# Kernel tuning notes

Hardware: AMD Instinct MI355X
Metric: run time of the kernel (lower is better)

The kernel has to match this reference:

```python
import jax, jax.numpy as jnp
import numpy as np

B, N, D = 4, 1024, 1024   # batch, seq (x and context must match), model dim
H, DH = 16, 64            # heads, dim_head; inner_dim = H*DH = 1024
INNER = H * DH
EPS = 1e-5


def setup_inputs() -> dict:
    key = jax.random.key(0)
    ks = jax.random.split(key, 12)
    s = 0.02
    return {
        "x": jax.random.normal(ks[0], (B, N, D), dtype=jnp.float32),
        "context": jax.random.normal(ks[1], (B, N, D), dtype=jnp.float32),
        # weights stored as [in, out] (torch Linear weight transposed)
        "W_qk": jax.random.normal(ks[2], (D, INNER), dtype=jnp.float32) * s,
        "W_cqk": jax.random.normal(ks[3], (D, INNER), dtype=jnp.float32) * s,
        "W_v": jax.random.normal(ks[4], (D, INNER), dtype=jnp.float32) * s,
        "W_cv": jax.random.normal(ks[5], (D, INNER), dtype=jnp.float32) * s,
        "W_out": jax.random.normal(ks[6], (INNER, D), dtype=jnp.float32) * s,
        "b_out": jax.random.normal(ks[7], (D,), dtype=jnp.float32) * s,
        "W_cout": jax.random.normal(ks[8], (INNER, D), dtype=jnp.float32) * s,
        "b_cout": jax.random.normal(ks[9], (D,), dtype=jnp.float32) * s,
        "gamma": jnp.ones((D,), dtype=jnp.float32),
        "beta": jnp.zeros((D,), dtype=jnp.float32),
    }


def _split_heads(t):  # [b, n, h*d] -> [b, h, n, d]
    b, n, _ = t.shape
    return t.reshape(b, n, H, DH).transpose(0, 2, 1, 3)


def _merge_heads(t):  # [b, h, n, d] -> [b, n, h*d]
    b, h, n, d = t.shape
    return t.transpose(0, 2, 1, 3).reshape(b, n, h * d)


def _layernorm(y, gamma, beta):
    mu = jnp.mean(y, axis=-1, keepdims=True)
    var = jnp.var(y, axis=-1, keepdims=True)
    return gamma * (y - mu) * jax.lax.rsqrt(var + EPS) + beta


def reference(x, context, W_qk, W_cqk, W_v, W_cv, W_out, b_out, W_cout, b_cout, gamma, beta):
    scale = DH ** -0.5
    res = x + context                       # residual (requires identical shapes)
    # prenorm=False -> identity norms; dropout=0; talking_heads=False -> identity
    qk = _split_heads(x @ W_qk)             # [b,h,i,d]
    v = _split_heads(x @ W_v)               # [b,h,i,d]
    cqk = _split_heads(context @ W_cqk)     # [b,h,j,d]
    cv = _split_heads(context @ W_cv)       # [b,h,j,d]

    sim = jnp.einsum('bhid,bhjd->bhij', qk, cqk) * scale  # shared similarity
    attn = jax.nn.softmax(sim, axis=-1)      # row softmax (x attends to context)
    context_attn = jax.nn.softmax(sim, axis=-2)  # column softmax (context attends to x)

    out = jnp.einsum('bhij,bhjd->bhid', attn, cv)          # [b,h,i,d]
    context_out = jnp.einsum('bhji,bhjd->bhid', context_attn, v)  # [b,h,i,d]

    out = _merge_heads(out) @ W_out + b_out
    context_out = _merge_heads(context_out) @ W_cout + b_cout
    return _layernorm(out + context_out, gamma, beta) + res
```

## Files before the change

kernel.cpp:

```cpp
#include <hip/hip_runtime.h>
#include <hip/hip_bf16.h>

typedef unsigned short u16;
typedef __bf16 bf16x8 __attribute__((ext_vector_type(8)));
typedef float   f32x4 __attribute__((ext_vector_type(4)));
typedef u16     u16x8 __attribute__((ext_vector_type(8)));
typedef u16     u16x4 __attribute__((ext_vector_type(4)));

#define DEV static __device__ __forceinline__

DEV float bf2f(u16 b) { unsigned int u = ((unsigned int)b) << 16; return __builtin_bit_cast(float, u); }
DEV u16   f2bf(float f) { return __builtin_bit_cast(u16, (__bf16)f); }
DEV bf16x8 ldb(const u16* p) { return __builtin_bit_cast(bf16x8, *(const u16x8*)p); }

DEV f32x4 mfma_bf16(bf16x8 a, bf16x8 b, f32x4 c) {
  return __builtin_amdgcn_mfma_f32_16x16x32_bf16(a, b, c, 0, 0, 0);
}

DEV void gl16(const u16* g, u16* l) {
  __builtin_amdgcn_global_load_lds((const __attribute__((address_space(1))) unsigned int*)g,
                                   (__attribute__((address_space(3))) unsigned int*)l,
                                   16, 0, 0);
}

#define BAR_VM4()  asm volatile("s_waitcnt vmcnt(4)\ns_barrier" ::: "memory")
#define BAR_VM0()  asm volatile("s_waitcnt vmcnt(0)\ns_barrier" ::: "memory")
#define BAR_LG()   asm volatile("s_waitcnt lgkmcnt(0)\ns_barrier" ::: "memory")
#define BAR_FULL() asm volatile("s_waitcnt vmcnt(0) lgkmcnt(0)\ns_barrier" ::: "memory")

__global__ __launch_bounds__(256) void detect_dtype(const u16* x, int* flag) {
  int tid = threadIdx.x;
  u16 lo = x[tid * 2];
  float v = bf2f(lo);
  float av = fabsf(v);
  bool plaus = (av > 1e-4f && av < 50.f);
  __shared__ int cnt;
  if (tid == 0) cnt = 0;
  __syncthreads();
  if (plaus) atomicAdd(&cnt, 1);
  __syncthreads();
  if (tid == 0) *flag = (cnt >= 128) ? 1 : 0;
}

struct Cv2 { const void* s[2]; u16* d[2]; };
__global__ __launch_bounds__(256) void convert_big(Cv2 p, const int* flagp) {
  int fl = *flagp;
  const void* src = p.s[blockIdx.z];
  u16* dst = p.d[blockIdx.z];
  size_t i = ((size_t)blockIdx.x * 256 + threadIdx.x) * 8;
  if (fl) {
    *(u16x8*)(dst + i) = *(const u16x8*)((const u16*)src + i);
  } else {
    const float* s = (const float*)src + i;
    u16x8 o;
#pragma unroll
    for (int k = 0; k < 8; ++k) o[k] = f2bf(s[k]);
    *(u16x8*)(dst + i) = o;
  }
}

struct Sm4 { const void* s[4]; u16* d[4]; };
__global__ __launch_bounds__(256) void convert_smalls(Sm4 p, const int* flagp) {
  int fl = *flagp;
  const void* src = p.s[blockIdx.x];
  u16* dst = p.d[blockIdx.x];
  int i = threadIdx.x * 4;
#pragma unroll
  for (int k = 0; k < 4; ++k)
    dst[i + k] = fl ? ((const u16*)src)[i + k] : f2bf(((const float*)src)[i + k]);
}

struct T6 { const void* s[6]; u16* d[6]; };

__global__ __launch_bounds__(256) void transpose6(T6 t, const int* flagp) {
  int fl = *flagp;
  __shared__ u16 tile[64 * 72];
  const void* src = t.s[blockIdx.z];
  u16* dst = t.d[blockIdx.z];
  int x0 = blockIdx.x * 64, y0 = blockIdx.y * 64;
  int tid = threadIdx.x;
  int r8 = tid >> 3, ch = tid & 7;

#pragma unroll
  for (int half = 0; half < 2; ++half) {
    int rl = r8 + half * 32;
    size_t si = (size_t)(y0 + rl) * 1024 + x0 + ch * 8;
    u16x8 v;
    if (fl) {
      v = *(const u16x8*)((const u16*)src + si);
    } else {
      const float* s = (const float*)src + si;
      float4 a = *(const float4*)s, b2 = *(const float4*)(s + 4);
      v[0]=f2bf(a.x); v[1]=f2bf(a.y); v[2]=f2bf(a.z); v[3]=f2bf(a.w);
      v[4]=f2bf(b2.x); v[5]=f2bf(b2.y); v[6]=f2bf(b2.z); v[7]=f2bf(b2.w);
    }
    int pr = rl ^ (ch << 3);
#pragma unroll
    for (int k = 0; k < 8; ++k)
      tile[(ch * 8 + k) * 72 + pr] = v[k];
  }
  __syncthreads();
#pragma unroll
  for (int half = 0; half < 2; ++half) {
    int dr = r8 + half * 32;
    int pch = ch ^ ((dr >> 3) & 7);
    u16x8 v = *(const u16x8*)(tile + dr * 72 + pch * 8);
    *(u16x8*)(dst + (size_t)(x0 + dr) * 1024 + y0 + ch * 8) = v;
  }
}

struct Proj4 { const u16* A[4]; const u16* Bt[4]; u16* C[4]; int mode[4]; };

__global__ __launch_bounds__(512, 2) void gemm_proj(Proj4 p) {
  const int K = 1024, Nn = 1024;
  const u16* A  = p.A[blockIdx.z];
  const u16* Bt = p.Bt[blockIdx.z];
  u16* C = p.C[blockIdx.z];
  int mode = p.mode[blockIdx.z];

  __shared__ __align__(16) u16 As[2][256 * 64];
  __shared__ __align__(16) u16 Bs[2][256 * 64];

  int tid = threadIdx.x, lane = tid & 63, w = tid >> 6;
  int wm = w >> 2, wn = w & 3;
  int q4 = lane >> 4, c = lane & 15;

  int bid = blockIdx.y * 4 + blockIdx.x;
  int wg  = (bid & 7) * 8 + (bid >> 3);
  int m0 = (wg >> 2) * 256, n0 = (wg & 3) * 256;

  int srow = w * 8 + (lane >> 3);
  int scol = ((lane & 7) ^ (lane >> 3)) * 8;
  const u16* pAg = A  + (size_t)(m0 + srow) * K + scol;
  const u16* pBg = Bt + (size_t)(n0 + srow) * K + scol;
  int sdst = (w * 8) * 64;

  int xo0 = ((0 * 4 + q4) ^ (c & 7)) * 8;
  int xo1 = ((1 * 4 + q4) ^ (c & 7)) * 8;

  f32x4 acc[8][4] = {};

#define STAGE256(pb, kt)                                                    \
  { int ko = (kt) * 64;                                                     \
    _Pragma("unroll") for (int s = 0; s < 4; ++s) {                         \
      gl16(pAg + (size_t)s * 64 * 1024 + ko, As[pb] + s * 4096 + sdst);     \
      gl16(pBg + (size_t)s * 64 * 1024 + ko, Bs[pb] + s * 4096 + sdst);     \
    } }

#define COMP256(pb)                                                         \
  { bf16x8 bq[4][2];                                                        \
    _Pragma("unroll") for (int j = 0; j < 4; ++j) {                         \
      int rb = (wn * 64 + j * 16 + c) * 64;                                 \
      bq[j][0] = ldb(Bs[pb] + rb + xo0);                                    \
      bq[j][1] = ldb(Bs[pb] + rb + xo1);                                    \
    }                                                                       \
    _Pragma("unroll") for (int f = 0; f < 4; ++f) {                         \
      bf16x8 aq[2][2];                                                      \
      _Pragma("unroll") for (int ii = 0; ii < 2; ++ii) {                    \
        int ra = (wm * 128 + (f * 2 + ii) * 16 + c) * 64;                   \
        aq[ii][0] = ldb(As[pb] + ra + xo0);                                 \
        aq[ii][1] = ldb(As[pb] + ra + xo1);                                 \
      }                                                                     \
      __builtin_amdgcn_s_setprio(1);                                        \
      _Pragma("unroll") for (int ii = 0; ii < 2; ++ii)                      \
        _Pragma("unroll") for (int j = 0; j < 4; ++j) {                     \
          acc[f*2+ii][j] = mfma_bf16(aq[ii][0], bq[j][0], acc[f*2+ii][j]);  \
          acc[f*2+ii][j] = mfma_bf16(aq[ii][1], bq[j][1], acc[f*2+ii][j]);  \
        }                                                                   \
      __builtin_amdgcn_s_setprio(0);                                        \
    } }

  STAGE256(0, 0);
  BAR_VM0();
  for (int t = 0; t < 16; t += 2) {
    STAGE256(1, t + 1);
    COMP256(0);
    BAR_FULL();
    if (t + 2 < 16) STAGE256(0, t + 2);
    COMP256(1);
    BAR_FULL();
  }
#undef STAGE256
#undef COMP256

  if (mode == 0) {
#pragma unroll
    for (int i = 0; i < 8; ++i) {
      int mrow = m0 + wm * 128 + i * 16 + q4 * 4;
#pragma unroll
      for (int j = 0; j < 4; ++j) {
        int col = n0 + wn * 64 + j * 16 + c;
#pragma unroll
        for (int r = 0; r < 4; ++r)
          C[(size_t)(mrow + r) * Nn + col] = f2bf(acc[i][j][r]);
      }
    }
  } else {
    int bidx = m0 >> 10;
#pragma unroll
    for (int i = 0; i < 8; ++i) {
      int mrow = m0 + wm * 128 + i * 16 + q4 * 4;
      int jj = mrow & 1023;
#pragma unroll
      for (int j = 0; j < 4; ++j) {
        int col = n0 + wn * 64 + j * 16 + c;
        int h = col >> 6, dh = col & 63;
        u16x4 pk;
#pragma unroll
        for (int r = 0; r < 4; ++r) pk[r] = f2bf(acc[i][j][r]);
        *(u16x4*)(C + ((size_t)((bidx * 16 + h) * 64 + dh)) * 1024 + jj) = pk;
      }
    }
  }
}

struct FAz { const u16* Q[2]; const u16* Kp[2]; const u16* Vp[2]; u16* O[2]; };

__global__ __launch_bounds__(256) void flash_attn(FAz fa) {
  int flat = blockIdx.x;
  int i0 = (flat >> 7) * 128;
  int grp = flat & 127;
  int z = grp >> 6;
  int bh = grp & 63;
  const u16* Q  = fa.Q[z];
  const u16* Kg = fa.Kp[z];
  const u16* Vt = fa.Vp[z];
  u16* O = fa.O[z];

  int b = bh >> 4, h = bh & 15;
  int tid = threadIdx.x, lane = tid & 63, w = tid >> 6;
  int q4 = lane >> 4, c = lane & 15;

  __shared__ __align__(16) u16 Ks[64 * 64];
  __shared__ __align__(16) u16 Vs[64 * 64];
  __shared__ __align__(16) u16 Ps[4][2][16 * 72];

  bf16x8 qf[2][2];
#pragma unroll
  for (int g = 0; g < 2; ++g) {
    const size_t qoff = ((size_t)(b * 1024 + i0 + g * 64 + w * 16 + c)) * 1024 + h * 64 + q4 * 8;
    qf[g][0] = ldb(Q + qoff);
    qf[g][1] = ldb(Q + qoff + 32);
  }

  f32x4 of[2][4] = {};
  f32x4 lacc[2] = {};
  bf16x8 ones;
#pragma unroll
  for (int k = 0; k < 8; ++k) ones[k] = (__bf16)1.0f;

  int jr = tid >> 2, seg = (tid & 3) * 16;
  const u16* krow_base = Kg + ((size_t)(b * 1024 + jr)) * 1024 + h * 64 + seg;
  const u16* vrow_base = Vt + ((size_t)((b * 16 + h) * 64 + jr)) * 1024 + seg;

  int ch0 = (tid & 3) * 2, jrx = jr & 7;
  int wa0 = jr * 64 + ((ch0)     ^ jrx) * 8;
  int wa1 = jr * 64 + ((ch0 + 1) ^ jrx) * 8;
  int xA = (q4 ^ (c & 7)) * 8;
  int xB = xA ^ 32;

  const float C2 = 0.125f * 1.4426950408889634f;

  u16x8 kv0 = *(const u16x8*)(krow_base);
  u16x8 kv1 = *(const u16x8*)(krow_base + 8);
  u16x8 vv0 = *(const u16x8*)(vrow_base);
  u16x8 vv1 = *(const u16x8*)(vrow_base + 8);

  for (int j0 = 0; j0 < 1024; j0 += 64) {
    __syncthreads();
    *(u16x8*)(Ks + wa0) = kv0;
    *(u16x8*)(Ks + wa1) = kv1;
    *(u16x8*)(Vs + wa0) = vv0;
    *(u16x8*)(Vs + wa1) = vv1;
    __syncthreads();

    if (j0 + 64 < 1024) {
      const u16* ks = krow_base + (size_t)(j0 + 64) * 1024;
      kv0 = *(const u16x8*)(ks);
      kv1 = *(const u16x8*)(ks + 8);
      const u16* vs = vrow_base + j0 + 64;
      vv0 = *(const u16x8*)(vs);
      vv1 = *(const u16x8*)(vs + 8);
    }

    f32x4 sf[2][4] = {};
    __builtin_amdgcn_s_setprio(1);
#pragma unroll
    for (int jc = 0; jc < 4; ++jc) {
      int rk = (jc * 16 + c) * 64;
      bf16x8 k0f = ldb(Ks + rk + xA);
      bf16x8 k1f = ldb(Ks + rk + xB);
#pragma unroll
      for (int g = 0; g < 2; ++g) {
        sf[g][jc] = mfma_bf16(k0f, qf[g][0], sf[g][jc]);
        sf[g][jc] = mfma_bf16(k1f, qf[g][1], sf[g][jc]);
      }
    }
    __builtin_amdgcn_s_setprio(0);

#pragma unroll
    for (int g = 0; g < 2; ++g)
#pragma unroll
      for (int jc = 0; jc < 4; ++jc) {
        u16x4 pk;
#pragma unroll
        for (int r = 0; r < 4; ++r)
          pk[r] = f2bf(__builtin_amdgcn_exp2f(sf[g][jc][r] * C2));
        *(u16x4*)(Ps[w][g] + c * 72 + jc * 16 + q4 * 4) = pk;
      }

    asm volatile("s_waitcnt lgkmcnt(0)" ::: "memory");

    bf16x8 pf[2][2];
#pragma unroll
    for (int g = 0; g < 2; ++g) {
      pf[g][0] = ldb(Ps[w][g] + c * 72 + q4 * 8);
      pf[g][1] = ldb(Ps[w][g] + c * 72 + 32 + q4 * 8);
      lacc[g] = mfma_bf16(pf[g][0], ones, lacc[g]);
      lacc[g] = mfma_bf16(pf[g][1], ones, lacc[g]);
    }

    __builtin_amdgcn_s_setprio(1);
#pragma unroll
    for (int dc = 0; dc < 4; ++dc) {
      int rv = (dc * 16 + c) * 64;
      bf16x8 v0f = ldb(Vs + rv + xA);
      bf16x8 v1f = ldb(Vs + rv + xB);
#pragma unroll
      for (int g = 0; g < 2; ++g) {
        of[g][dc] = mfma_bf16(pf[g][0], v0f, of[g][dc]);
        of[g][dc] = mfma_bf16(pf[g][1], v1f, of[g][dc]);
      }
    }
    __builtin_amdgcn_s_setprio(0);
  }

#pragma unroll
  for (int g = 0; g < 2; ++g) {
    float inv[4];
#pragma unroll
    for (int r = 0; r < 4; ++r) inv[r] = 1.0f / lacc[g][r];
#pragma unroll
    for (int dc = 0; dc < 4; ++dc) {
      int col = h * 64 + dc * 16 + c;
#pragma unroll
      for (int r = 0; r < 4; ++r) {
        int irow = i0 + g * 64 + w * 16 + q4 * 4 + r;
        O[((size_t)(b * 1024 + irow)) * 1024 + col] = f2bf(of[g][dc][r] * inv[r]);
      }
    }
  }
}

__global__ __launch_bounds__(256) void gemm_final(const u16* A1, const u16* B1t,
                                                  const u16* A2, const u16* B2t,
                                                  const u16* b1, const u16* b2,
                                                  float* Y) {
  const int K = 1024, Nn = 1024;
  __shared__ __align__(16) u16 As[2][128 * 32];
  __shared__ __align__(16) u16 Bs[2][128 * 32];

  int tid = threadIdx.x, lane = tid & 63, w = tid >> 6;
  int wm = w & 1, wn = w >> 1;
  int q4 = lane >> 4, c = lane & 15;

  int bid = blockIdx.y * 8 + blockIdx.x;
  int wg  = (bid & 7) * 32 + (bid >> 3);
  int m0 = (wg >> 3) * 128, n0 = (wg & 7) * 128;

  int r0 = w * 32 + (lane >> 2);
  int cc = (lane & 3) ^ ((lane >> 3) & 3);
  const u16* A1p = A1  + (size_t)(m0 + r0) * K + cc * 8;
  const u16* A2p = A2  + (size_t)(m0 + r0) * K + cc * 8;
  const u16* B1p = B1t + (size_t)(n0 + r0) * K + cc * 8;
  const u16* B2p = B2t + (size_t)(n0 + r0) * K + cc * 8;
  int qs = (q4 ^ ((c >> 1) & 3)) * 8;

  f32x4 acc[4][4] = {};

#define STAGE_F(buf, kk)                                          \
  { const u16* Ap = ((kk) < 32) ? A1p : A2p;                      \
    const u16* Bp = ((kk) < 32) ? B1p : B2p;                      \
    int k0_ = ((kk) & 31) * 32;                                   \
    gl16(Ap + k0_,          As[buf] + w * 1024);                  \
    gl16(Ap + 16 * K + k0_, As[buf] + w * 1024 + 512);            \
    gl16(Bp + k0_,          Bs[buf] + w * 1024);                  \
    gl16(Bp + 16 * K + k0_, Bs[buf] + w * 1024 + 512); }

#define COMP_F(buf)                                               \
  { bf16x8 af[4], bfr[4];                                         \
    _Pragma("unroll") for (int i = 0; i < 4; ++i)                 \
      af[i]  = ldb(As[buf] + (wm * 64 + i * 16 + c) * 32 + qs);   \
    _Pragma("unroll") for (int j = 0; j < 4; ++j)                 \
      bfr[j] = ldb(Bs[buf] + (wn * 64 + j * 16 + c) * 32 + qs);   \
    _Pragma("unroll") for (int i = 0; i < 4; ++i)                 \
      _Pragma("unroll") for (int j = 0; j < 4; ++j)               \
        acc[i][j] = mfma_bf16(af[i], bfr[j], acc[i][j]); }

  STAGE_F(0, 0);
  for (int t = 0; t < 62; t += 2) {
    STAGE_F(1, t + 1);
    BAR_VM4();
    COMP_F(0);
    BAR_LG();
    STAGE_F(0, t + 2);
    BAR_VM4();
    COMP_F(1);
    BAR_LG();
  }
  STAGE_F(1, 63);
  BAR_VM4();
  COMP_F(0);
  BAR_LG();
  BAR_VM0();
  COMP_F(1);
#undef STAGE_F
#undef COMP_F

#pragma unroll
  for (int i = 0; i < 4; ++i) {
    int mrow = m0 + wm * 64 + i * 16 + q4 * 4;
#pragma unroll
    for (int j = 0; j < 4; ++j) {
      int col = n0 + wn * 64 + j * 16 + c;
      float bias = bf2f(b1[col]) + bf2f(b2[col]);
#pragma unroll
      for (int r = 0; r < 4; ++r)
        Y[(size_t)(mrow + r) * Nn + col] = acc[i][j][r] + bias;
    }
  }
}

__global__ __launch_bounds__(256) void ln_res(const float* Y, const u16* gamma, const u16* beta,
                                              const void* x, const void* ctx, void* out,
                                              const int* flagp) {
  int fl = *flagp;
  int row = blockIdx.x;
  int tid = threadIdx.x;
  const float* y = Y + (size_t)row * 1024;
  float4 v = *(const float4*)(y + tid * 4);
  float s  = v.x + v.y + v.z + v.w;
  float s2 = v.x * v.x + v.y * v.y + v.z * v.z + v.w * v.w;
#pragma unroll
  for (int off = 1; off < 64; off <<= 1) { s += __shfl_xor(s, off); s2 += __shfl_xor(s2, off); }
  __shared__ float red[8];
  int w = tid >> 6, lane = tid & 63;
  if (lane == 0) { red[w] = s; red[w + 4] = s2; }
  __syncthreads();
  float S  = red[0] + red[1] + red[2] + red[3];
  float S2 = red[4] + red[5] + red[6] + red[7];
  float mu  = S * (1.0f / 1024.0f);
  float var = S2 * (1.0f / 1024.0f) - mu * mu;
  float rs = rsqrtf(var + 1e-5f);
  size_t base = (size_t)row * 1024 + tid * 4;
  u16x4 gv = *(const u16x4*)(gamma + tid * 4);
  u16x4 bv = *(const u16x4*)(beta + tid * 4);
  float xr[4], cr[4];
  if (fl) {
    u16x4 xv = *(const u16x4*)((const u16*)x + base);
    u16x4 cv = *(const u16x4*)((const u16*)ctx + base);
#pragma unroll
    for (int k = 0; k < 4; ++k) { xr[k] = bf2f(xv[k]); cr[k] = bf2f(cv[k]); }
  } else {
    float4 xv = *(const float4*)((const float*)x + base);
    float4 cv = *(const float4*)((const float*)ctx + base);
    xr[0] = xv.x; xr[1] = xv.y; xr[2] = xv.z; xr[3] = xv.w;
    cr[0] = cv.x; cr[1] = cv.y; cr[2] = cv.z; cr[3] = cv.w;
  }
  float vv[4] = {v.x, v.y, v.z, v.w};
  float o[4];
#pragma unroll
  for (int k = 0; k < 4; ++k)
    o[k] = bf2f(gv[k]) * (vv[k] - mu) * rs + bf2f(bv[k]) + xr[k] + cr[k];
  if (fl) {
    u16x4 ov;
#pragma unroll
    for (int k = 0; k < 4; ++k) ov[k] = f2bf(o[k]);
    *(u16x4*)((u16*)out + base) = ov;
  } else {
    *(float4*)((float*)out + base) = make_float4(o[0], o[1], o[2], o[3]);
  }
}

__global__ __launch_bounds__(256) void sentinel(u16* out) {
  size_t i = ((size_t)blockIdx.x * 256 + threadIdx.x) * 8;
  u16 v = f2bf(12345.0f);
  u16x8 o = {v, v, v, v, v, v, v, v};
  *(u16x8*)(out + i) = o;
}

extern "C" void kernel_launch(void* const* d_in, const int* in_sizes, int n_in,
                              void* d_out, int out_size, void* d_ws, size_t ws_size,
                              hipStream_t stream) {
  (void)in_sizes; (void)n_in; (void)out_size;
  const size_t MB = 1024 * 1024;
  const size_t NEED = 61 * MB;
  if (ws_size < NEED) {
    sentinel<<<2048, 256, 0, stream>>>((u16*)d_out);
    return;
  }

  char* ws = (char*)d_ws;
  u16* wt[6];
  for (int i = 0; i < 6; ++i) wt[i] = (u16*)(ws + (size_t)i * 2 * MB);
  u16* xc   = (u16*)(ws + 12 * MB);
  u16* cc   = (u16*)(ws + 20 * MB);
  u16* qk   = (u16*)(ws + 28 * MB);
  u16* cqk  = (u16*)(ws + 36 * MB);
  u16* vt   = (u16*)(ws + 44 * MB);
  u16* cvt  = (u16*)(ws + 52 * MB);
  u16* oa   = (u16*)(ws + 0);
  u16* ca   = (u16*)(ws + 12 * MB);
  float* y  = (float*)(ws + 28 * MB);
  int* flag = (int*)(ws + 60 * MB);
  u16* b1c  = (u16*)(ws + 60 * MB + 4096);
  u16* b2c  = (u16*)(ws + 60 * MB + 8192);
  u16* gc   = (u16*)(ws + 60 * MB + 12288);
  u16* bc   = (u16*)(ws + 60 * MB + 16384);

  detect_dtype<<<1, 256, 0, stream>>>((const u16*)d_in[0], flag);

  Cv2 cv;
  cv.s[0] = d_in[0]; cv.d[0] = xc;
  cv.s[1] = d_in[1]; cv.d[1] = cc;
  convert_big<<<dim3(2048, 1, 2), 256, 0, stream>>>(cv, flag);

  Sm4 sm;
  sm.s[0] = d_in[7]; sm.d[0] = b1c;
  sm.s[1] = d_in[9]; sm.d[1] = b2c;
  sm.s[2] = d_in[10]; sm.d[2] = gc;
  sm.s[3] = d_in[11]; sm.d[3] = bc;
  convert_smalls<<<4, 256, 0, stream>>>(sm, flag);

  T6 t;
  t.s[0] = d_in[2]; t.d[0] = wt[0];
  t.s[1] = d_in[3]; t.d[1] = wt[1];
  t.s[2] = d_in[4]; t.d[2] = wt[2];
  t.s[3] = d_in[5]; t.d[3] = wt[3];
  t.s[4] = d_in[6]; t.d[4] = wt[4];
  t.s[5] = d_in[8]; t.d[5] = wt[5];
  transpose6<<<dim3(16, 16, 6), 256, 0, stream>>>(t, flag);

  Proj4 p;
  p.A[0] = xc; p.Bt[0] = wt[0]; p.C[0] = qk;  p.mode[0] = 0;
  p.A[1] = cc; p.Bt[1] = wt[1]; p.C[1] = cqk; p.mode[1] = 0;
  p.A[2] = xc; p.Bt[2] = wt[2]; p.C[2] = vt;  p.mode[2] = 1;
  p.A[3] = cc; p.Bt[3] = wt[3]; p.C[3] = cvt; p.mode[3] = 1;
  gemm_proj<<<dim3(4, 16, 4), 512, 0, stream>>>(p);

  FAz fa;
  fa.Q[0] = qk;  fa.Kp[0] = cqk; fa.Vp[0] = cvt; fa.O[0] = oa;
  fa.Q[1] = cqk; fa.Kp[1] = qk;  fa.Vp[1] = vt;  fa.O[1] = ca;
  flash_attn<<<dim3(1024), 256, 0, stream>>>(fa);

  gemm_final<<<dim3(8, 32), 256, 0, stream>>>(oa, wt[4], ca, wt[5], b1c, b2c, y);

  ln_res<<<4096, 256, 0, stream>>>(y, gc, bc, d_in[0], d_in[1], d_out, flag);
}
```

Before: 253.9 us.

## Keep attention probabilities in registers via 16x16x16 MFMA and skip bf16 copy

The flash attention kernel no longer stages exponentiated scores through a shared-memory P buffer. The score accumulator layout is fed directly as the A operand of 16x16x16 bf16 MFMAs against V fragments read in a matching layout. This removes LDS writes and reads and a waitcnt per tile, at the cost of twice as many smaller MFMA issues. Separately, when inputs are already bf16 the conversion kernel exits early and the projection GEMM reads the raw inputs directly, skipping one copy pass.

```diff
diff --git a/kernel.cpp b/kernel.cpp
--- a/kernel.cpp
+++ b/kernel.cpp
@@ -6,6 +6,7 @@
 typedef float   f32x4 __attribute__((ext_vector_type(4)));
 typedef u16     u16x8 __attribute__((ext_vector_type(8)));
 typedef u16     u16x4 __attribute__((ext_vector_type(4)));
+typedef short   s16x4 __attribute__((ext_vector_type(4)));
 
 #define DEV static __device__ __forceinline__
 
@@ -15,6 +16,16 @@
 
 DEV f32x4 mfma_bf16(bf16x8 a, bf16x8 b, f32x4 c) {
   return __builtin_amdgcn_mfma_f32_16x16x32_bf16(a, b, c, 0, 0, 0);
+}
+
+DEV f32x4 mfma16(s16x4 a, s16x4 b, f32x4 c) {
+#if __has_builtin(__builtin_amdgcn_mfma_f32_16x16x16bf16_1k)
+  return __builtin_amdgcn_mfma_f32_16x16x16bf16_1k(a, b, c, 0, 0, 0);
+#else
+  f32x4 d = c;
+  asm volatile("v_mfma_f32_16x16x16_bf16 %0, %1, %2, %0" : "+v"(d) : "v"(a), "v"(b));
+  return d;
+#endif
 }
 
 DEV void gl16(const u16* g, u16* l) {
@@ -45,18 +56,15 @@
 struct Cv2 { const void* s[2]; u16* d[2]; };
 __global__ __launch_bounds__(256) void convert_big(Cv2 p, const int* flagp) {
   int fl = *flagp;
+  if (fl) return;
   const void* src = p.s[blockIdx.z];
   u16* dst = p.d[blockIdx.z];
   size_t i = ((size_t)blockIdx.x * 256 + threadIdx.x) * 8;
-  if (fl) {
-    *(u16x8*)(dst + i) = *(const u16x8*)((const u16*)src + i);
-  } else {
-    const float* s = (const float*)src + i;
-    u16x8 o;
-#pragma unroll
-    for (int k = 0; k < 8; ++k) o[k] = f2bf(s[k]);
-    *(u16x8*)(dst + i) = o;
-  }
+  const float* s = (const float*)src + i;
+  u16x8 o;
+#pragma unroll
+  for (int k = 0; k < 8; ++k) o[k] = f2bf(s[k]);
+  *(u16x8*)(dst + i) = o;
 }
 
 struct Sm4 { const void* s[4]; u16* d[4]; };
@@ -109,11 +117,12 @@
   }
 }
 
-struct Proj4 { const u16* A[4]; const u16* Bt[4]; u16* C[4]; int mode[4]; };
-
-__global__ __launch_bounds__(512, 2) void gemm_proj(Proj4 p) {
+struct Proj4 { const u16* A[4]; const u16* Araw[4]; const u16* Bt[4]; u16* C[4]; int mode[4]; };
+
+__global__ __launch_bounds__(512, 2) void gemm_proj(Proj4 p, const int* flagp) {
   const int K = 1024, Nn = 1024;
-  const u16* A  = p.A[blockIdx.z];
+  int fl = *flagp;
+  const u16* A  = fl ? p.Araw[blockIdx.z] : p.A[blockIdx.z];
   const u16* Bt = p.Bt[blockIdx.z];
   u16* C = p.C[blockIdx.z];
   int mode = p.mode[blockIdx.z];
@@ -233,7 +242,6 @@
 
   __shared__ __align__(16) u16 Ks[64 * 64];
   __shared__ __align__(16) u16 Vs[64 * 64];
-  __shared__ __align__(16) u16 Ps[4][2][16 * 72];
 
   bf16x8 qf[2][2];
 #pragma unroll
@@ -245,9 +253,9 @@
 
   f32x4 of[2][4] = {};
   f32x4 lacc[2] = {};
-  bf16x8 ones;
-#pragma unroll
-  for (int k = 0; k < 8; ++k) ones[k] = (__bf16)1.0f;
+  s16x4 ones4;
+#pragma unroll
+  for (int k = 0; k < 4; ++k) ones4[k] = (short)0x3F80;
 
   int jr = tid >> 2, seg = (tid & 3) * 16;
   const u16* krow_base = Kg + ((size_t)(b * 1024 + jr)) * 1024 + h * 64 + seg;
@@ -258,6 +266,7 @@
   int wa1 = jr * 64 + ((ch0 + 1) ^ jrx) * 8;
   int xA = (q4 ^ (c & 7)) * 8;
   int xB = xA ^ 32;
+  int q4h = q4 >> 1, q4l4 = (q4 & 1) * 4;
 
   const float C2 = 0.125f * 1.4426950408889634f;
 
@@ -299,40 +308,27 @@
     __builtin_amdgcn_s_setprio(0);
 
 #pragma unroll
-    for (int g = 0; g < 2; ++g)
-#pragma unroll
-      for (int jc = 0; jc < 4; ++jc) {
+    for (int jc = 0; jc < 4; ++jc) {
+      u16x4 vb[4];
+#pragma unroll
+      for (int dc = 0; dc < 4; ++dc) {
+        int row = dc * 16 + c;
+        int ch = 2 * jc + q4h;
+        vb[dc] = *(const u16x4*)(Vs + row * 64 + ((ch ^ (row & 7)) * 8) + q4l4);
+      }
+#pragma unroll
+      for (int g = 0; g < 2; ++g) {
         u16x4 pk;
 #pragma unroll
         for (int r = 0; r < 4; ++r)
           pk[r] = f2bf(__builtin_amdgcn_exp2f(sf[g][jc][r] * C2));
-        *(u16x4*)(Ps[w][g] + c * 72 + jc * 16 + q4 * 4) = pk;
+        s16x4 pa = __builtin_bit_cast(s16x4, pk);
+        lacc[g] = mfma16(pa, ones4, lacc[g]);
+#pragma unroll
+        for (int dc = 0; dc < 4; ++dc)
+          of[g][dc] = mfma16(pa, __builtin_bit_cast(s16x4, vb[dc]), of[g][dc]);
       }
-
-    asm volatile("s_waitcnt lgkmcnt(0)" ::: "memory");
-
-    bf16x8 pf[2][2];
-#pragma unroll
-    for (int g = 0; g < 2; ++g) {
-      pf[g][0] = ldb(Ps[w][g] + c * 72 + q4 * 8);
-      pf[g][1] = ldb(Ps[w][g] + c * 72 + 32 + q4 * 8);
-      lacc[g] = mfma_bf16(pf[g][0], ones, lacc[g]);
-      lacc[g] = mfma_bf16(pf[g][1], ones, lacc[g]);
-    }
-
-    __builtin_amdgcn_s_setprio(1);
-#pragma unroll
-    for (int dc = 0; dc < 4; ++dc) {
-      int rv = (dc * 16 + c) * 64;
-      bf16x8 v0f = ldb(Vs + rv + xA);
-      bf16x8 v1f = ldb(Vs + rv + xB);
-#pragma unroll
-      for (int g = 0; g < 2; ++g) {
-        of[g][dc] = mfma_bf16(pf[g][0], v0f, of[g][dc]);
-        of[g][dc] = mfma_bf16(pf[g][1], v1f, of[g][dc]);
-      }
-    }
-    __builtin_amdgcn_s_setprio(0);
+    }
   }
 
 #pragma unroll
@@ -542,11 +538,11 @@
   transpose6<<<dim3(16, 16, 6), 256, 0, stream>>>(t, flag);
 
   Proj4 p;
-  p.A[0] = xc; p.Bt[0] = wt[0]; p.C[0] = qk;  p.mode[0] = 0;
-  p.A[1] = cc; p.Bt[1] = wt[1]; p.C[1] = cqk; p.mode[1] = 0;
-  p.A[2] = xc; p.Bt[2] = wt[2]; p.C[2] = vt;  p.mode[2] = 1;
-  p.A[3] = cc; p.Bt[3] = wt[3]; p.C[3] = cvt; p.mode[3] = 1;
-  gemm_proj<<<dim3(4, 16, 4), 512, 0, stream>>>(p);
+  p.A[0] = xc; p.Araw[0] = (const u16*)d_in[0]; p.Bt[0] = wt[0]; p.C[0] = qk;  p.mode[0] = 0;
+  p.A[1] = cc; p.Araw[1] = (const u16*)d_in[1]; p.Bt[1] = wt[1]; p.C[1] = cqk; p.mode[1] = 0;
+  p.A[2] = xc; p.Araw[2] = (const u16*)d_in[0]; p.Bt[2] = wt[2]; p.C[2] = vt;  p.mode[2] = 1;
+  p.A[3] = cc; p.Araw[3] = (const u16*)d_in[1]; p.Bt[3] = wt[3]; p.C[3] = cvt; p.mode[3] = 1;
+  gemm_proj<<<dim3(4, 16, 4), 512, 0, stream>>>(p, flag);
 
   FAz fa;
   fa.Q[0] = qk;  fa.Kp[0] = cqk; fa.Vp[0] = cvt; fa.O[0] = oa;
```

After: 262.9 us. 1.04x slower.
